# Kernel tuning notes

Hardware: AMD Instinct MI355X
Metric: run time of the kernel (lower is better)

## Reference

```python
import jax, jax.numpy as jnp
import numpy as np

N_NODES = 50000
N_EDGES = 800000
D = 64
N_GRAPHS = 64


def setup_inputs() -> dict:
    key = jax.random.key(0)
    ks = jax.random.split(key, 8)
    scale = 1.0 / np.sqrt(D)
    x = jax.random.normal(ks[0], (N_NODES, D), dtype=jnp.float32)
    edge_index = jax.random.randint(ks[1], (2, N_EDGES), 0, N_NODES, dtype=jnp.int32)
    batch = jnp.sort(jax.random.randint(ks[2], (N_NODES,), 0, N_GRAPHS, dtype=jnp.int32))
    Wq = jax.random.normal(ks[3], (D, D), dtype=jnp.float32) * scale
    Wk = jax.random.normal(ks[4], (D, D), dtype=jnp.float32) * scale
    Wv = jax.random.normal(ks[5], (D, D), dtype=jnp.float32) * scale
    Ws = jax.random.normal(ks[6], (D, D), dtype=jnp.float32) * scale
    z = jnp.zeros((D,), dtype=jnp.float32)
    return {"x": x, "edge_index": edge_index, "batch": batch,
            "Wq": Wq, "bq": z, "Wk": Wk, "bk": z, "Wv": Wv, "bv": z,
            "Ws": Ws, "bs": z}


def reference(x, edge_index, batch, Wq, bq, Wk, bk, Wv, bv, Ws, bs):
    # TransformerConv(heads=1, concat=True, root_weight=True), then ReLU, then global_mean_pool
    src = edge_index[0]  # source node j (message sender)
    dst = edge_index[1]  # target node i (message receiver)
    q = x @ Wq + bq      # [N, D]
    k = x @ Wk + bk      # [N, D]
    v = x @ Wv + bv      # [N, D]
    inv_sqrt_d = jnp.float32(1.0 / np.sqrt(D))
    # per-edge attention logits: (q_i . k_j) / sqrt(D)
    logits = jnp.sum(q[dst] * k[src], axis=-1) * inv_sqrt_d  # [E]
    # segment softmax over incoming edges of each target node
    seg_max = jax.ops.segment_max(logits, dst, num_segments=N_NODES)  # [N]
    ex = jnp.exp(logits - seg_max[dst])                               # [E]
    denom = jax.ops.segment_sum(ex, dst, num_segments=N_NODES)        # [N]
    alpha = ex / denom[dst]                                           # [E]
    # scatter-add weighted values to target nodes
    agg = jax.ops.segment_sum(alpha[:, None] * v[src], dst, num_segments=N_NODES)  # [N, D]
    out = agg + (x @ Ws + bs)  # root/skip connection
    out = jax.nn.relu(out)
    # global mean pool per graph
    sums = jax.ops.segment_sum(out, batch, num_segments=N_GRAPHS)            # [G, D]
    cnt = jax.ops.segment_sum(jnp.ones((N_NODES,), out.dtype), batch, num_segments=N_GRAPHS)
    return sums / jnp.maximum(cnt, 1.0)[:, None]
```

## Files before the change

kernel.cpp:

```cpp
#include <hip/hip_runtime.h>
#include <hip/hip_bf16.h>

#define D 64
#define NG 64
#define CAP 64
#define NB 196
#define BCAP 5120

typedef short bf16x8 __attribute__((ext_vector_type(8)));
typedef float f32x4  __attribute__((ext_vector_type(4)));
typedef unsigned short u16x8 __attribute__((ext_vector_type(8)));

__device__ __forceinline__ float b2f(unsigned short u){
  return __uint_as_float(((unsigned)u) << 16);
}
__device__ __forceinline__ unsigned short f2bu(float f){
  return __builtin_bit_cast(unsigned short, __float2bfloat16(f));
}

template<int C>
__device__ __forceinline__ float dppadd(float x){
  int t = __builtin_amdgcn_update_dpp(0, __float_as_int(x), C, 0xf, 0xf, true);
  return x + __int_as_float(t);
}

__global__ __launch_bounds__(256) void k_wprep(
    const float* __restrict__ Wq, const float* __restrict__ Wk,
    const float* __restrict__ Wv, const float* __restrict__ Ws,
    short* __restrict__ fragw, int* __restrict__ zptr, int zn)
{
  for (int i = blockIdx.x*256 + threadIdx.x; i < zn; i += 8*256) zptr[i] = 0;

  const int m    = blockIdx.x >> 1;
  const int kh   = blockIdx.x & 1;
  const int ct   = threadIdx.x >> 6;
  const int lane = threadIdx.x & 63;
  const int r16  = lane & 15;
  const int kg   = lane >> 4;
  const float* Wm = (m==0) ? Wq : (m==1) ? Wk : (m==2) ? Wv : Ws;
  bf16x8 hi, lo;
  #pragma unroll
  for (int j = 0; j < 8; ++j){
    float wv = Wm[(32*kh + 8*kg + j)*D + 16*ct + r16];
    unsigned short hb = f2bu(wv);
    hi[j] = (short)hb;
    lo[j] = (short)f2bu(wv - b2f(hb));
  }
  int fi = ct*2 + kh;
  *(bf16x8*)(fragw + ((size_t)(fi*2+0)*256 + m*64 + lane)*8) = hi;
  *(bf16x8*)(fragw + ((size_t)(fi*2+1)*256 + m*64 + lane)*8) = lo;
}

__global__ __launch_bounds__(256) void k_fused(
    const int* __restrict__ esrc, const int* __restrict__ edst,
    int* __restrict__ bcnt, unsigned* __restrict__ bedge, int E, int nChunk,
    int nSplit,
    const float* __restrict__ x, const short* __restrict__ fragw,
    const float* __restrict__ bq, const float* __restrict__ bk,
    const float* __restrict__ bv, const float* __restrict__ bs,
    unsigned short* __restrict__ qb, __hip_bfloat16* __restrict__ kb,
    __hip_bfloat16* __restrict__ vb, float* __restrict__ sp, int N)
{
  __shared__ int hist[NB], gpos[NB], cur[NB];

  if ((int)blockIdx.x < nSplit){
    const int tid = threadIdx.x;
    if (tid < NB){ hist[tid] = 0; cur[tid] = 0; }
    __syncthreads();
    const int c0 = blockIdx.x * nChunk;
    const int c1 = min(c0 + nChunk, E);
    for (int e = c0 + tid; e < c1; e += 256)
      atomicAdd(&hist[edst[e] >> 8], 1);
    __syncthreads();
    if (tid < NB && hist[tid] > 0)
      gpos[tid] = atomicAdd(bcnt + tid*16, hist[tid]);
    __syncthreads();
    for (int e = c0 + tid; e < c1; e += 256){
      int d = edst[e];
      int b = d >> 8;
      int p = gpos[b] + atomicAdd(&cur[b], 1);
      if (p < BCAP)
        bedge[(size_t)b*BCAP + p] = (unsigned)esrc[e] | ((unsigned)(d & 255) << 16);
    }
    return;
  }

  const int lane = threadIdx.x & 63;
  const int w    = threadIdx.x >> 6;
  const int r16  = lane & 15;
  const int kg   = lane >> 4;

  const float* bm = (w==0) ? bq : (w==1) ? bk : (w==2) ? bv : bs;

  bf16x8 wh[4][2], wl[4][2];
  #pragma unroll
  for (int fi = 0; fi < 8; ++fi){
    wh[fi>>1][fi&1] = *(const bf16x8*)(fragw + ((size_t)(fi*2+0)*256 + w*64 + lane)*8);
    wl[fi>>1][fi&1] = *(const bf16x8*)(fragw + ((size_t)(fi*2+1)*256 + w*64 + lane)*8);
  }
  float bias[4];
  #pragma unroll
  for (int ct = 0; ct < 4; ++ct) bias[ct] = bm[16*ct + r16];

  const int nStrip = N >> 4;
  const int s0 = (blockIdx.x - nSplit) * 2;
  #pragma unroll
  for (int it = 0; it < 2; ++it){
    const int strip = s0 + it;
    if (strip >= nStrip) break;
    const int R0 = strip << 4;
    const float* xp = x + (size_t)(R0 + r16)*D + 8*kg;
    float4 a0 = *(const float4*)(xp);
    float4 a1 = *(const float4*)(xp + 4);
    float4 a2 = *(const float4*)(xp + 32);
    float4 a3 = *(const float4*)(xp + 36);

    bf16x8 xh[2], xl[2];
    {
      float t;
      unsigned short hb;
      #define PK(kh, j, val) t=(val); hb=f2bu(t); xh[kh][j]=(short)hb; \
                             xl[kh][j]=(short)f2bu(t - b2f(hb));
      PK(0,0,a0.x) PK(0,1,a0.y) PK(0,2,a0.z) PK(0,3,a0.w)
      PK(0,4,a1.x) PK(0,5,a1.y) PK(0,6,a1.z) PK(0,7,a1.w)
      PK(1,0,a2.x) PK(1,1,a2.y) PK(1,2,a2.z) PK(1,3,a2.w)
      PK(1,4,a3.x) PK(1,5,a3.y) PK(1,6,a3.z) PK(1,7,a3.w)
      #undef PK
    }

    #pragma unroll
    for (int ct = 0; ct < 4; ++ct){
      f32x4 acc = {bias[ct], bias[ct], bias[ct], bias[ct]};
      #pragma unroll
      for (int kh = 0; kh < 2; ++kh){
        acc = __builtin_amdgcn_mfma_f32_16x16x32_bf16(xh[kh], wh[ct][kh], acc, 0,0,0);
        acc = __builtin_amdgcn_mfma_f32_16x16x32_bf16(xh[kh], wl[ct][kh], acc, 0,0,0);
        acc = __builtin_amdgcn_mfma_f32_16x16x32_bf16(xl[kh], wh[ct][kh], acc, 0,0,0);
      }
      #pragma unroll
      for (int i = 0; i < 4; ++i){
        size_t o = (size_t)(R0 + 4*kg + i)*D + 16*ct + r16;
        if (w == 0)      qb[o] = f2bu(acc[i]);
        else if (w == 1) ((unsigned short*)kb)[o] = f2bu(acc[i]);
        else if (w == 2) ((unsigned short*)vb)[o] = f2bu(acc[i]);
        else             sp[o] = acc[i];
      }
    }
  }
}

__global__ __launch_bounds__(256) void k_bsort(
    const int* __restrict__ bcnt, const unsigned* __restrict__ bedge,
    int* __restrict__ cnt, unsigned short* __restrict__ slots, int N)
{
  __shared__ int cur[256];
  const int tid = threadIdx.x;
  const int b = blockIdx.x;
  cur[tid] = 0;
  __syncthreads();
  const int n = min(bcnt[b*16], BCAP);
  for (int i = tid; i < n; i += 256){
    unsigned e = bedge[(size_t)b*BCAP + i];
    int dl = e >> 16;
    int p = atomicAdd(&cur[dl], 1);
    if (p < CAP) slots[(size_t)(b*256 + dl)*CAP + p] = (unsigned short)(e & 0xFFFF);
  }
  __syncthreads();
  int dst = b*256 + tid;
  if (dst < N) cnt[dst] = cur[tid];
}

__global__ __launch_bounds__(256) void k_attend(
    const unsigned short* __restrict__ qb, const __hip_bfloat16* __restrict__ kb,
    const __hip_bfloat16* __restrict__ vb, float* __restrict__ sp,
    const int* __restrict__ cnt, const unsigned short* __restrict__ slots, int N)
{
  int node = blockIdx.x*4 + (threadIdx.x >> 6);
  if (node >= N) return;
  const int lane = threadIdx.x & 63;
  const int grp  = lane >> 3;
  const int gl   = lane & 7;

  u16x8 q8 = *(const u16x8*)(qb + (size_t)node*D + 8*gl);
  float qf0=b2f(q8[0]), qf1=b2f(q8[1]), qf2=b2f(q8[2]), qf3=b2f(q8[3]);
  float qf4=b2f(q8[4]), qf5=b2f(q8[5]), qf6=b2f(q8[6]), qf7=b2f(q8[7]);

  int dg = min(cnt[node], CAP);
  int p0 = node*CAP;

  float den = 0.f;
  float4 aa = {0,0,0,0}, ab = {0,0,0,0};

  const unsigned short* ku = (const unsigned short*)kb;
  const unsigned short* vu = (const unsigned short*)vb;

  int sidx = (lane < dg) ? (int)slots[p0 + lane] : 0;
  int T = (dg + 7) >> 3;
  #pragma unroll 2
  for (int t = 0; t < T; ++t){
    int ei  = grp + 8*t;
    int eis = min(ei, dg - 1);
    int s = __shfl(sidx, eis, 64);
    if (ei < dg){
      u16x8 k8 = *(const u16x8*)(ku + (size_t)s*D + 8*gl);
      float p = qf0*b2f(k8[0]) + qf1*b2f(k8[1])
              + qf2*b2f(k8[2]) + qf3*b2f(k8[3])
              + qf4*b2f(k8[4]) + qf5*b2f(k8[5])
              + qf6*b2f(k8[6]) + qf7*b2f(k8[7]);
      p = dppadd<0xB1>(p);
      p = dppadd<0x4E>(p);
      p = dppadd<0x141>(p);
      float ex = __expf(fminf(p * 0.125f, 60.f));
      u16x8 v8 = *(const u16x8*)(vu + (size_t)s*D + 8*gl);
      den += ex;
      aa.x = fmaf(ex, b2f(v8[0]), aa.x);
      aa.y = fmaf(ex, b2f(v8[1]), aa.y);
      aa.z = fmaf(ex, b2f(v8[2]), aa.z);
      aa.w = fmaf(ex, b2f(v8[3]), aa.w);
      ab.x = fmaf(ex, b2f(v8[4]), ab.x);
      ab.y = fmaf(ex, b2f(v8[5]), ab.y);
      ab.z = fmaf(ex, b2f(v8[6]), ab.z);
      ab.w = fmaf(ex, b2f(v8[7]), ab.w);
    }
  }

  #define MRG(v) v = dppadd<0x128>(v); \
                 v += __shfl_xor(v, 16, 64); \
                 v += __shfl_xor(v, 32, 64);
  MRG(den)
  MRG(aa.x) MRG(aa.y) MRG(aa.z) MRG(aa.w)
  MRG(ab.x) MRG(ab.y) MRG(ab.z) MRG(ab.w)
  #undef MRG

  if (grp == 0){
    float4* spp = (float4*)(sp + (size_t)node*D);
    float4 s4a = spp[2*gl], s4b = spp[2*gl+1];
    float4 oa, ob;
    if (dg > 0){
      float inv = 1.f/den;
      oa.x = fmaf(aa.x, inv, s4a.x); oa.y = fmaf(aa.y, inv, s4a.y);
      oa.z = fmaf(aa.z, inv, s4a.z); oa.w = fmaf(aa.w, inv, s4a.w);
      ob.x = fmaf(ab.x, inv, s4b.x); ob.y = fmaf(ab.y, inv, s4b.y);
      ob.z = fmaf(ab.w ? ab.z : ab.z, 0.f, 0.f);
      ob.z = fmaf(ab.z, inv, s4b.z); ob.w = fmaf(ab.w, inv, s4b.w);
    } else {
      oa = s4a; ob = s4b;
    }
    oa.x = fmaxf(oa.x, 0.f); oa.y = fmaxf(oa.y, 0.f);
    oa.z = fmaxf(oa.z, 0.f); oa.w = fmaxf(oa.w, 0.f);
    ob.x = fmaxf(ob.x, 0.f); ob.y = fmaxf(ob.y, 0.f);
    ob.z = fmaxf(ob.z, 0.f); ob.w = fmaxf(ob.w, 0.f);
    spp[2*gl]   = oa;
    spp[2*gl+1] = ob;
  }
}

__global__ __launch_bounds__(256) void k_pool(
    const float* __restrict__ rows, const int* __restrict__ batch,
    float* __restrict__ gsum, float* __restrict__ gcnt, int N, int rpw)
{
  const int lane = threadIdx.x & 63;
  const int wid  = threadIdx.x >> 6;
  int wi = blockIdx.x*4 + wid;
  int start = wi * rpw;
  if (start >= N) return;
  int end = min(start + rpw, N);

  float acc = 0.f, c = 0.f;
  int gcur = batch[start];
  #pragma unroll 4
  for (int row = start; row < end; ++row){
    int g = batch[row];
    float val = rows[(size_t)row*D + lane];
    if (g != gcur){
      atomicAdd(gsum + (size_t)gcur*D + lane, acc);
      if (lane == 0) atomicAdd(gcnt + gcur, c);
      acc = 0.f; c = 0.f; gcur = g;
    }
    acc += val;
    c += 1.f;
  }
  atomicAdd(gsum + (size_t)gcur*D + lane, acc);
  if (lane == 0) atomicAdd(gcnt + gcur, c);
}

__global__ __launch_bounds__(256) void k_final(
    const float* __restrict__ gsum, const float* __restrict__ gcnt,
    float* __restrict__ out, int n)
{
  int i = blockIdx.x*256 + threadIdx.x;
  if (i >= n) return;
  int g = i >> 6;
  out[i] = gsum[i] / fmaxf(gcnt[g], 1.0f);
}

extern "C" void kernel_launch(void* const* d_in, const int* in_sizes, int n_in,
                              void* d_out, int out_size, void* d_ws, size_t ws_size,
                              hipStream_t stream)
{
  const float* x   = (const float*)d_in[0];
  const int*  ei   = (const int*)d_in[1];
  const int*  batch= (const int*)d_in[2];
  const float* Wq  = (const float*)d_in[3];
  const float* bq  = (const float*)d_in[4];
  const float* Wk  = (const float*)d_in[5];
  const float* bk  = (const float*)d_in[6];
  const float* Wv  = (const float*)d_in[7];
  const float* bv  = (const float*)d_in[8];
  const float* Ws  = (const float*)d_in[9];
  const float* bs  = (const float*)d_in[10];
  float* out = (float*)d_out;

  const int N = in_sizes[0] / D;
  const int E = in_sizes[1] / 2;
  const int* esrc = ei;
  const int* edst = ei + E;

  float* ws = (float*)d_ws;
  size_t off = 0;
  unsigned short* qb = (unsigned short*)(ws + off); off += (size_t)N*D/2;
  __hip_bfloat16* kb = (__hip_bfloat16*)(ws + off); off += (size_t)N*D/2;
  __hip_bfloat16* vb = (__hip_bfloat16*)(ws + off); off += (size_t)N*D/2;
  float* sp   = ws + off; off += (size_t)N*D;
  int*   bcnt = (int*)(ws + off);  off += (size_t)NB*16;
  float* gsum = ws + off; off += (size_t)NG*D;
  float* gcnt = ws + off; off += NG;
  int*   cnt  = (int*)(ws + off);  off += N;
  unsigned* bedge = (unsigned*)(ws + off); off += (size_t)NB*BCAP;
  unsigned short* slots = (unsigned short*)(ws + off); off += (size_t)N*CAP/2;
  short* fragw = (short*)(ws + off); off += 16*256*8/2;

  const int zn = NB*16 + NG*D + NG;
  const int nChunk = (E + 255) / 256;
  const int nSplit = 256;
  const int nLin   = ((N >> 4) + 1) / 2;

  k_wprep <<<8, 256, 0, stream>>>(Wq, Wk, Wv, Ws, fragw, bcnt, zn);
  k_fused <<<nSplit + nLin, 256, 0, stream>>>(esrc, edst, bcnt, bedge, E, nChunk,
                                              nSplit, x, fragw, bq, bk, bv, bs,
                                              qb, kb, vb, sp, N);
  k_bsort <<<NB, 256, 0, stream>>>(bcnt, bedge, cnt, slots, N);
  k_attend<<<(N+3)/4, 256, 0, stream>>>(qb, kb, vb, sp, cnt, slots, N);
  const int rpw = 32;
  int nwaves = (N + rpw - 1) / rpw;
  k_pool <<<(nwaves+3)/4, 256, 0, stream>>>(sp, batch, gsum, gcnt, N, rpw);
  k_final<<<(NG*D+255)/256, 256, 0, stream>>>(gsum, gcnt, out, NG*D);
}
```

Measured before the change: 101.3 us.

## Process two nodes per wave in attention and fuse final division into pool

The attention kernel now gives each wavefront two target nodes and interleaves their K/V gathers, so more independent memory loads are in flight per wave. Edge-count divergence is handled by masking the exponent to zero rather than branching, which means the shorter node issues redundant loads up to the longer node's degree. The pool kernel adds a last-block-done counter, so the final mean division happens in that block and one kernel launch is removed. It relies on a threadfence plus atomic counter, and the counter is zeroed in the existing prep kernel.

```diff
diff --git a/kernel.cpp b/kernel.cpp
--- a/kernel.cpp
+++ b/kernel.cpp
@@ -175,123 +175,143 @@
     const __hip_bfloat16* __restrict__ vb, float* __restrict__ sp,
     const int* __restrict__ cnt, const unsigned short* __restrict__ slots, int N)
 {
-  int node = blockIdx.x*4 + (threadIdx.x >> 6);
-  if (node >= N) return;
-  const int lane = threadIdx.x & 63;
+  const int tid  = threadIdx.x;
+  const int lane = tid & 63;
   const int grp  = lane >> 3;
   const int gl   = lane & 7;
 
-  u16x8 q8 = *(const u16x8*)(qb + (size_t)node*D + 8*gl);
-  float qf0=b2f(q8[0]), qf1=b2f(q8[1]), qf2=b2f(q8[2]), qf3=b2f(q8[3]);
-  float qf4=b2f(q8[4]), qf5=b2f(q8[5]), qf6=b2f(q8[6]), qf7=b2f(q8[7]);
-
-  int dg = min(cnt[node], CAP);
-  int p0 = node*CAP;
-
-  float den = 0.f;
-  float4 aa = {0,0,0,0}, ab = {0,0,0,0};
+  int n0 = blockIdx.x*8 + (tid >> 6)*2;
+  int n1 = n0 + 1;
+  if (n1 >= N) return;
+
+  u16x8 qA = *(const u16x8*)(qb + (size_t)n0*D + 8*gl);
+  u16x8 qB = *(const u16x8*)(qb + (size_t)n1*D + 8*gl);
+
+  int dg0 = min(cnt[n0], CAP), dg1 = min(cnt[n1], CAP);
+  int dgm0 = max(dg0-1, 0),    dgm1 = max(dg1-1, 0);
+  int sidx0 = (lane < dg0) ? (int)slots[(size_t)n0*CAP + lane] : 0;
+  int sidx1 = (lane < dg1) ? (int)slots[(size_t)n1*CAP + lane] : 0;
+
+  float den0 = 0.f, den1 = 0.f;
+  float4 aa0 = {0,0,0,0}, ab0 = {0,0,0,0};
+  float4 aa1 = {0,0,0,0}, ab1 = {0,0,0,0};
 
   const unsigned short* ku = (const unsigned short*)kb;
   const unsigned short* vu = (const unsigned short*)vb;
 
-  int sidx = (lane < dg) ? (int)slots[p0 + lane] : 0;
-  int T = (dg + 7) >> 3;
+  int T = max((dg0 + 7) >> 3, (dg1 + 7) >> 3);
   #pragma unroll 2
   for (int t = 0; t < T; ++t){
     int ei  = grp + 8*t;
-    int eis = min(ei, dg - 1);
-    int s = __shfl(sidx, eis, 64);
-    if (ei < dg){
-      u16x8 k8 = *(const u16x8*)(ku + (size_t)s*D + 8*gl);
-      float p = qf0*b2f(k8[0]) + qf1*b2f(k8[1])
-              + qf2*b2f(k8[2]) + qf3*b2f(k8[3])
-              + qf4*b2f(k8[4]) + qf5*b2f(k8[5])
-              + qf6*b2f(k8[6]) + qf7*b2f(k8[7]);
-      p = dppadd<0xB1>(p);
-      p = dppadd<0x4E>(p);
-      p = dppadd<0x141>(p);
-      float ex = __expf(fminf(p * 0.125f, 60.f));
-      u16x8 v8 = *(const u16x8*)(vu + (size_t)s*D + 8*gl);
-      den += ex;
-      aa.x = fmaf(ex, b2f(v8[0]), aa.x);
-      aa.y = fmaf(ex, b2f(v8[1]), aa.y);
-      aa.z = fmaf(ex, b2f(v8[2]), aa.z);
-      aa.w = fmaf(ex, b2f(v8[3]), aa.w);
-      ab.x = fmaf(ex, b2f(v8[4]), ab.x);
-      ab.y = fmaf(ex, b2f(v8[5]), ab.y);
-      ab.z = fmaf(ex, b2f(v8[6]), ab.z);
-      ab.w = fmaf(ex, b2f(v8[7]), ab.w);
-    }
+    int s0 = __shfl(sidx0, min(ei, dgm0), 64);
+    int s1 = __shfl(sidx1, min(ei, dgm1), 64);
+    u16x8 k80 = *(const u16x8*)(ku + (size_t)s0*D + 8*gl);
+    u16x8 k81 = *(const u16x8*)(ku + (size_t)s1*D + 8*gl);
+    u16x8 v80 = *(const u16x8*)(vu + (size_t)s0*D + 8*gl);
+    u16x8 v81 = *(const u16x8*)(vu + (size_t)s1*D + 8*gl);
+
+    float p0 = b2f(qA[0])*b2f(k80[0]) + b2f(qA[1])*b2f(k80[1])
+             + b2f(qA[2])*b2f(k80[2]) + b2f(qA[3])*b2f(k80[3])
+             + b2f(qA[4])*b2f(k80[4]) + b2f(qA[5])*b2f(k80[5])
+             + b2f(qA[6])*b2f(k80[6]) + b2f(qA[7])*b2f(k80[7]);
+    float p1 = b2f(qB[0])*b2f(k81[0]) + b2f(qB[1])*b2f(k81[1])
+             + b2f(qB[2])*b2f(k81[2]) + b2f(qB[3])*b2f(k81[3])
+             + b2f(qB[4])*b2f(k81[4]) + b2f(qB[5])*b2f(k81[5])
+             + b2f(qB[6])*b2f(k81[6]) + b2f(qB[7])*b2f(k81[7]);
+    p0 = dppadd<0xB1>(p0); p1 = dppadd<0xB1>(p1);
+    p0 = dppadd<0x4E>(p0); p1 = dppadd<0x4E>(p1);
+    p0 = dppadd<0x141>(p0); p1 = dppadd<0x141>(p1);
+
+    float ex0 = (ei < dg0) ? __expf(fminf(p0 * 0.125f, 60.f)) : 0.f;
+    float ex1 = (ei < dg1) ? __expf(fminf(p1 * 0.125f, 60.f)) : 0.f;
+    den0 += ex0; den1 += ex1;
+    aa0.x = fmaf(ex0, b2f(v80[0]), aa0.x); aa0.y = fmaf(ex0, b2f(v80[1]), aa0.y);
+    aa0.z = fmaf(ex0, b2f(v80[2]), aa0.z); aa0.w = fmaf(ex0, b2f(v80[3]), aa0.w);
+    ab0.x = fmaf(ex0, b2f(v80[4]), ab0.x); ab0.y = fmaf(ex0, b2f(v80[5]), ab0.y);
+    ab0.z = fmaf(ex0, b2f(v80[6]), ab0.z); ab0.w = fmaf(ex0, b2f(v80[7]), ab0.w);
+    aa1.x = fmaf(ex1, b2f(v81[0]), aa1.x); aa1.y = fmaf(ex1, b2f(v81[1]), aa1.y);
+    aa1.z = fmaf(ex1, b2f(v81[2]), aa1.z); aa1.w = fmaf(ex1, b2f(v81[3]), aa1.w);
+    ab1.x = fmaf(ex1, b2f(v81[4]), ab1.x); ab1.y = fmaf(ex1, b2f(v81[5]), ab1.y);
+    ab1.z = fmaf(ex1, b2f(v81[6]), ab1.z); ab1.w = fmaf(ex1, b2f(v81[7]), ab1.w);
   }
 
   #define MRG(v) v = dppadd<0x128>(v); \
                  v += __shfl_xor(v, 16, 64); \
                  v += __shfl_xor(v, 32, 64);
-  MRG(den)
-  MRG(aa.x) MRG(aa.y) MRG(aa.z) MRG(aa.w)
-  MRG(ab.x) MRG(ab.y) MRG(ab.z) MRG(ab.w)
+  MRG(den0) MRG(den1)
+  MRG(aa0.x) MRG(aa0.y) MRG(aa0.z) MRG(aa0.w)
+  MRG(ab0.x) MRG(ab0.y) MRG(ab0.z) MRG(ab0.w)
+  MRG(aa1.x) MRG(aa1.y) MRG(aa1.z) MRG(aa1.w)
+  MRG(ab1.x) MRG(ab1.y) MRG(ab1.z) MRG(ab1.w)
   #undef MRG
 
   if (grp == 0){
-    float4* spp = (float4*)(sp + (size_t)node*D);
-    float4 s4a = spp[2*gl], s4b = spp[2*gl+1];
-    float4 oa, ob;
-    if (dg > 0){
-      float inv = 1.f/den;
-      oa.x = fmaf(aa.x, inv, s4a.x); oa.y = fmaf(aa.y, inv, s4a.y);
-      oa.z = fmaf(aa.z, inv, s4a.z); oa.w = fmaf(aa.w, inv, s4a.w);
-      ob.x = fmaf(ab.x, inv, s4b.x); ob.y = fmaf(ab.y, inv, s4b.y);
-      ob.z = fmaf(ab.w ? ab.z : ab.z, 0.f, 0.f);
-      ob.z = fmaf(ab.z, inv, s4b.z); ob.w = fmaf(ab.w, inv, s4b.w);
-    } else {
-      oa = s4a; ob = s4b;
-    }
-    oa.x = fmaxf(oa.x, 0.f); oa.y = fmaxf(oa.y, 0.f);
-    oa.z = fmaxf(oa.z, 0.f); oa.w = fmaxf(oa.w, 0.f);
-    ob.x = fmaxf(ob.x, 0.f); ob.y = fmaxf(ob.y, 0.f);
-    ob.z = fmaxf(ob.z, 0.f); ob.w = fmaxf(ob.w, 0.f);
-    spp[2*gl]   = oa;
-    spp[2*gl+1] = ob;
+    #define WRITEBACK(node, dg, den, aa, ab)                                  \
+    {                                                                         \
+      float4* spp = (float4*)(sp + (size_t)(node)*D);                         \
+      float4 s4a = spp[2*gl], s4b = spp[2*gl+1];                              \
+      float4 oa, ob;                                                          \
+      if ((dg) > 0){                                                          \
+        float inv = 1.f/(den);                                                \
+        oa.x = fmaf((aa).x, inv, s4a.x); oa.y = fmaf((aa).y, inv, s4a.y);     \
+        oa.z = fmaf((aa).z, inv, s4a.z); oa.w = fmaf((aa).w, inv, s4a.w);     \
+        ob.x = fmaf((ab).x, inv, s4b.x); ob.y = fmaf((ab).y, inv, s4b.y);     \
+        ob.z = fmaf((ab).z, inv, s4b.z); ob.w = fmaf((ab).w, inv, s4b.w);     \
+      } else { oa = s4a; ob = s4b; }                                          \
+      oa.x = fmaxf(oa.x, 0.f); oa.y = fmaxf(oa.y, 0.f);                       \
+      oa.z = fmaxf(oa.z, 0.f); oa.w = fmaxf(oa.w, 0.f);                       \
+      ob.x = fmaxf(ob.x, 0.f); ob.y = fmaxf(ob.y, 0.f);                       \
+      ob.z = fmaxf(ob.z, 0.f); ob.w = fmaxf(ob.w, 0.f);                       \
+      spp[2*gl]   = oa;                                                       \
+      spp[2*gl+1] = ob;                                                       \
+    }
+    WRITEBACK(n0, dg0, den0, aa0, ab0)
+    WRITEBACK(n1, dg1, den1, aa1, ab1)
+    #undef WRITEBACK
   }
 }
 
 __global__ __launch_bounds__(256) void k_pool(
     const float* __restrict__ rows, const int* __restrict__ batch,
-    float* __restrict__ gsum, float* __restrict__ gcnt, int N, int rpw)
-{
-  const int lane = threadIdx.x & 63;
-  const int wid  = threadIdx.x >> 6;
+    float* __restrict__ gsum, float* __restrict__ gcnt,
+    int* __restrict__ done, float* __restrict__ out,
+    int N, int rpw, int nBlocks)
+{
+  __shared__ int lastd;
+  const int tid  = threadIdx.x;
+  const int lane = tid & 63;
+  const int wid  = tid >> 6;
   int wi = blockIdx.x*4 + wid;
   int start = wi * rpw;
-  if (start >= N) return;
-  int end = min(start + rpw, N);
-
-  float acc = 0.f, c = 0.f;
-  int gcur = batch[start];
-  #pragma unroll 4
-  for (int row = start; row < end; ++row){
-    int g = batch[row];
-    float val = rows[(size_t)row*D + lane];
-    if (g != gcur){
-      atomicAdd(gsum + (size_t)gcur*D + lane, acc);
-      if (lane == 0) atomicAdd(gcnt + gcur, c);
-      acc = 0.f; c = 0.f; gcur = g;
-    }
-    acc += val;
-    c += 1.f;
-  }
-  atomicAdd(gsum + (size_t)gcur*D + lane, acc);
-  if (lane == 0) atomicAdd(gcnt + gcur, c);
-}
-
-__global__ __launch_bounds__(256) void k_final(
-    const float* __restrict__ gsum, const float* __restrict__ gcnt,
-    float* __restrict__ out, int n)
-{
-  int i = blockIdx.x*256 + threadIdx.x;
-  if (i >= n) return;
-  int g = i >> 6;
-  out[i] = gsum[i] / fmaxf(gcnt[g], 1.0f);
+
+  if (start < N){
+    int end = min(start + rpw, N);
+    float acc = 0.f, c = 0.f;
+    int gcur = batch[start];
+    #pragma unroll 4
+    for (int row = start; row < end; ++row){
+      int g = batch[row];
+      float val = rows[(size_t)row*D + lane];
+      if (g != gcur){
+        atomicAdd(gsum + (size_t)gcur*D + lane, acc);
+        if (lane == 0) atomicAdd(gcnt + gcur, c);
+        acc = 0.f; c = 0.f; gcur = g;
+      }
+      acc += val;
+      c += 1.f;
+    }
+    atomicAdd(gsum + (size_t)gcur*D + lane, acc);
+    if (lane == 0) atomicAdd(gcnt + gcur, c);
+  }
+
+  __threadfence();
+  __syncthreads();
+  if (tid == 0) lastd = atomicAdd(done, 1);
+  __syncthreads();
+  if (lastd == nBlocks - 1){
+    for (int i = tid; i < NG*D; i += 256)
+      out[i] = gsum[i] / fmaxf(gcnt[i >> 6], 1.0f);
+  }
 }
 
 extern "C" void kernel_launch(void* const* d_in, const int* in_sizes, int n_in,
@@ -325,12 +345,13 @@
   int*   bcnt = (int*)(ws + off);  off += (size_t)NB*16;
   float* gsum = ws + off; off += (size_t)NG*D;
   float* gcnt = ws + off; off += NG;
+  int*   done = (int*)(ws + off);  off += 1;
   int*   cnt  = (int*)(ws + off);  off += N;
   unsigned* bedge = (unsigned*)(ws + off); off += (size_t)NB*BCAP;
   unsigned short* slots = (unsigned short*)(ws + off); off += (size_t)N*CAP/2;
   short* fragw = (short*)(ws + off); off += 16*256*8/2;
 
-  const int zn = NB*16 + NG*D + NG;
+  const int zn = NB*16 + NG*D + NG + 1;
   const int nChunk = (E + 255) / 256;
   const int nSplit = 256;
   const int nLin   = ((N >> 4) + 1) / 2;
@@ -340,9 +361,10 @@
                                               nSplit, x, fragw, bq, bk, bv, bs,
                                               qb, kb, vb, sp, N);
   k_bsort <<<NB, 256, 0, stream>>>(bcnt, bedge, cnt, slots, N);
-  k_attend<<<(N+3)/4, 256, 0, stream>>>(qb, kb, vb, sp, cnt, slots, N);
+  k_attend<<<(N+7)/8, 256, 0, stream>>>(qb, kb, vb, sp, cnt, slots, N);
   const int rpw = 32;
   int nwaves = (N + rpw - 1) / rpw;
-  k_pool <<<(nwaves+3)/4, 256, 0, stream>>>(sp, batch, gsum, gcnt, N, rpw);
-  k_final<<<(NG*D+255)/256, 256, 0, stream>>>(gsum, gcnt, out, NG*D);
-}
+  int nPool = (nwaves + 3) / 4;
+  k_pool <<<nPool, 256, 0, stream>>>(sp, batch, gsum, gcnt, done, out,
+                                     N, rpw, nPool);
+}
```

Measured after the change: 121.0 us. 19.5% more time.
